# Kernel tuning notes

Hardware: AMD Instinct MI355X
Metric: run time of the kernel (lower is better)

Reference implementation:

```python
import jax, jax.numpy as jnp
import numpy as np
import math

EMBED_DIM = 64

def setup_inputs() -> dict:
    key = jax.random.key(0)
    ks = jax.random.split(key, 9)
    B, S, H, E = 2, 2048, 8, EMBED_DIM
    f16 = jnp.float16
    inp = {
        'query': jax.random.normal(ks[0], (B, S, H, E), dtype=f16),
        'key':   jax.random.normal(ks[1], (B, S, H, E), dtype=f16),
        'value': jax.random.normal(ks[2], (B, S, H, E), dtype=f16),
        # Linear params (torch Linear: y = x @ W.T + b); W stored as [out,in]
        'Wq': (jax.random.normal(ks[3], (E, E), dtype=f16) / np.float16(math.sqrt(E))),
        'bq': jax.random.normal(ks[4], (E,), dtype=f16) * np.float16(0.02),
        'Wk': (jax.random.normal(ks[5], (E, E), dtype=f16) / np.float16(math.sqrt(E))),
        'bk': jax.random.normal(ks[6], (E,), dtype=f16) * np.float16(0.02),
        'Wv': (jax.random.normal(ks[7], (E, E), dtype=f16) / np.float16(math.sqrt(E))),
        'bv': jax.random.normal(ks[8], (E,), dtype=f16) * np.float16(0.02),
    }
    return inp

def reference(query, key, value, Wq, bq, Wk, bk, Wv, bv):
    # Linear projections on last dim, fused with permute(0,2,1,3): [B,S,H,E] -> [B,H,S,E]
    q = jnp.einsum('bshe,fe->bhsf', query, Wq) + bq
    k = jnp.einsum('bshe,fe->bhsf', key, Wk) + bk
    v = jnp.einsum('bshe,fe->bhsf', value, Wv) + bv
    scale = jnp.asarray(1.0 / math.sqrt(q.shape[-1]), dtype=q.dtype)
    q = q * scale
    # full attention matrix [B,H,S,S], fp16 matmul then fp32 softmax (faithful to source)
    scores = jnp.einsum('bhse,bhte->bhst', q, k).astype(jnp.float32)
    attn = jax.nn.softmax(scores, axis=-1).astype(jnp.float16)
    out = jnp.einsum('bhst,bhte->bhse', attn, v)
    return out
```

## Files before the change

kernel.cpp:

```cpp
#include <hip/hip_runtime.h>

#define S_LEN 2048
#define NH    8
#define EMB   64
#define BM    64
#define BN    64
#define NKT   (S_LEN / BN)
#define NSPLIT 3
#define PSTR  72
#define M_INIT  (-1.0e4f)
#define EXP_CLAMP (-80.0f)

typedef _Float16 half8   __attribute__((ext_vector_type(8)));
typedef _Float16 half4   __attribute__((ext_vector_type(4)));
typedef float    float4_t __attribute__((ext_vector_type(4)));
typedef float    float8_t __attribute__((ext_vector_type(8)));

__device__ inline half8 cvt8(const float* p) {
    float8_t f = *reinterpret_cast<const float8_t*>(p);
    half8 h;
    #pragma unroll
    for (int j = 0; j < 8; ++j) h[j] = (_Float16)f[j];
    return h;
}

__device__ inline void gload_lds16(const _Float16* g, _Float16* l) {
    __builtin_amdgcn_global_load_lds(
        (const __attribute__((address_space(1))) void*)g,
        (__attribute__((address_space(3))) void*)l, 16, 0, 0);
}

__global__ __launch_bounds__(256) void proj_q(
    const float* __restrict__ X, const float* __restrict__ W,
    const float* __restrict__ bias, float* __restrict__ Out)
{
    const int tid  = threadIdx.x;
    const int lane = tid & 63;
    const int wave = tid >> 6;
    const int l15  = lane & 15;
    const int quad = lane >> 4;
    const int gwave = blockIdx.x * 4 + wave;

    half8 wf[4][2];
    #pragma unroll
    for (int ft = 0; ft < 4; ++ft)
        #pragma unroll
        for (int ks = 0; ks < 2; ++ks)
            wf[ft][ks] = cvt8(W + (ft * 16 + l15) * 64 + ks * 32 + quad * 8);
    float bv[4];
    #pragma unroll
    for (int ft = 0; ft < 4; ++ft) bv[ft] = bias[ft * 16 + l15];

    #pragma unroll
    for (int rt2 = 0; rt2 < 2; ++rt2) {
        const int rt = gwave * 2 + rt2;
        const int arow = rt * 16 + l15;
        half8 xf[2];
        #pragma unroll
        for (int ks = 0; ks < 2; ++ks)
            xf[ks] = cvt8(X + (long)arow * 64 + ks * 32 + quad * 8);
        float4_t acc[4];
        #pragma unroll
        for (int ft = 0; ft < 4; ++ft) {
            acc[ft] = (float4_t){0.f, 0.f, 0.f, 0.f};
            #pragma unroll
            for (int ks = 0; ks < 2; ++ks)
                acc[ft] = __builtin_amdgcn_mfma_f32_16x16x32_f16(
                    xf[ks], wf[ft][ks], acc[ft], 0, 0, 0);
        }
        #pragma unroll
        for (int r = 0; r < 4; ++r) {
            const int row = rt * 16 + quad * 4 + r;
            const int b = row >> 14;
            const int s = (row >> 3) & 2047;
            const int h = row & 7;
            const long orow = ((long)(b * NH + h) * S_LEN + s) * EMB;
            #pragma unroll
            for (int ft = 0; ft < 4; ++ft) {
                const _Float16 v =
                    (_Float16)(acc[ft][r] + bv[ft]) * (_Float16)0.125f;
                Out[orow + ft * 16 + l15] = (float)v;
            }
        }
    }
}

__global__ __launch_bounds__(256) void proj_kv(
    const float* __restrict__ k_in, const float* __restrict__ v_in,
    const float* __restrict__ Wk, const float* __restrict__ bk,
    const float* __restrict__ Wv, const float* __restrict__ bv_,
    _Float16* __restrict__ KT8, _Float16* __restrict__ VT8)
{
    const int seg = blockIdx.x >> 8;
    const int bid = blockIdx.x & 255;
    const float* X    = seg ? v_in : k_in;
    const float* W    = seg ? Wv : Wk;
    const float* bias = seg ? bv_ : bk;

    const int tid  = threadIdx.x;
    const int lane = tid & 63;
    const int wave = tid >> 6;
    const int l15  = lane & 15;
    const int quad = lane >> 4;
    const int gwave = bid * 4 + wave;

    half8 wf[4][2];
    #pragma unroll
    for (int ft = 0; ft < 4; ++ft)
        #pragma unroll
        for (int ks = 0; ks < 2; ++ks)
            wf[ft][ks] = cvt8(W + (ft * 16 + l15) * 64 + ks * 32 + quad * 8);
    float bv[4];
    #pragma unroll
    for (int ft = 0; ft < 4; ++ft) bv[ft] = bias[ft * 16 + l15];

    #pragma unroll
    for (int rt2 = 0; rt2 < 2; ++rt2) {
        const int rt = gwave * 2 + rt2;
        const int arow = rt * 16 + l15;
        half8 xf[2];
        #pragma unroll
        for (int ks = 0; ks < 2; ++ks)
            xf[ks] = cvt8(X + (long)arow * 64 + ks * 32 + quad * 8);
        float4_t acc[4];
        #pragma unroll
        for (int ft = 0; ft < 4; ++ft) {
            acc[ft] = (float4_t){0.f, 0.f, 0.f, 0.f};
            #pragma unroll
            for (int ks = 0; ks < 2; ++ks)
                acc[ft] = __builtin_amdgcn_mfma_f32_16x16x32_f16(
                    xf[ks], wf[ft][ks], acc[ft], 0, 0, 0);
        }
        #pragma unroll
        for (int r = 0; r < 4; ++r) {
            const int row = rt * 16 + quad * 4 + r;
            const int b = row >> 14;
            const int s = (row >> 3) & 2047;
            const int h = row & 7;
            const int bh = b * NH + h;
            #pragma unroll
            for (int ft = 0; ft < 4; ++ft) {
                const _Float16 v = (_Float16)(acc[ft][r] + bv[ft]);
                const int f = ft * 16 + l15;
                if (seg == 0)
                    KT8[(((long)bh * 8 + (f >> 3)) * S_LEN + s) * 8 + (f & 7)] = v;
                else
                    VT8[(((long)bh * 256 + (s >> 3)) * 64 + f) * 8 + (s & 7)] = v;
            }
        }
    }
}

__global__ __launch_bounds__(256, 6) void attn_part(
    const _Float16* __restrict__ KT, const _Float16* __restrict__ VT,
    const float* __restrict__ Qbuf,
    _Float16* __restrict__ p0, _Float16* __restrict__ p1,
    _Float16* __restrict__ p2, float* __restrict__ stats)
{
    __shared__ __align__(16) _Float16 Kb[8 * 64 * 8];
    __shared__ __align__(16) _Float16 Vb[8 * 64 * 8];
    __shared__ __align__(16) _Float16 Pl[4][16 * PSTR];

    const int tid  = threadIdx.x;
    const int lane = tid & 63;
    const int wave = tid >> 6;
    const int l15  = lane & 15;
    const int quad = lane >> 4;
    const int bx   = blockIdx.x;
    const int bh   = bx / (32 * NSPLIT);
    const int rem  = bx % (32 * NSPLIT);
    const int qt   = rem / NSPLIT;
    const int sp   = rem % NSPLIT;
    const long base = (long)bh * S_LEN * EMB;
    const int qrow0 = qt * BM + wave * 16;

    const _Float16* kg = KT + (long)bh * 8 * S_LEN * 8;

    half8 qf[2];
    #pragma unroll
    for (int ks = 0; ks < 2; ++ks)
        qf[ks] = cvt8(Qbuf + base + (long)(qrow0 + l15) * EMB + ks * 32 + quad * 8);

    float4_t o[4];
    #pragma unroll
    for (int et = 0; et < 4; ++et) o[et] = (float4_t){0.f, 0.f, 0.f, 0.f};
    float m_run = M_INIT, l_run = 0.f;

    const int kb = (sp * NKT) / NSPLIT, ke = ((sp + 1) * NKT) / NSPLIT;
    for (int kt = kb; kt < ke; ++kt) {
        if (kt > kb) __syncthreads();
        const int t0 = kt * BN;
        #pragma unroll
        for (int rr = 0; rr < 2; ++rr) {
            const int u = rr * 256 + tid;
            const int ec = u >> 6, tl = u & 63;
            gload_lds16(kg + ((long)ec * S_LEN + t0 + tl) * 8, Kb + u * 8);
        }
        const _Float16* vg = VT + ((long)bh * 256 + (t0 >> 3)) * 512;
        #pragma unroll
        for (int rr = 0; rr < 2; ++rr) {
            const int u = rr * 256 + tid;
            gload_lds16(vg + u * 8, Vb + u * 8);
        }
        __syncthreads();

        float4_t sacc[4];
        #pragma unroll
        for (int nt = 0; nt < 4; ++nt) sacc[nt] = (float4_t){0.f, 0.f, 0.f, 0.f};
        #pragma unroll
        for (int nt = 0; nt < 4; ++nt)
            #pragma unroll
            for (int ks = 0; ks < 2; ++ks) {
                half8 kf = *reinterpret_cast<const half8*>(
                    Kb + (ks * 4 + quad) * 512 + (nt * 16 + l15) * 8);
                sacc[nt] = __builtin_amdgcn_mfma_f32_16x16x32_f16(
                    kf, qf[ks], sacc[nt], 0, 0, 0);
            }

        float mx = sacc[0][0];
        #pragma unroll
        for (int nt = 0; nt < 4; ++nt)
            #pragma unroll
            for (int r = 0; r < 4; ++r) mx = fmaxf(mx, sacc[nt][r]);
        mx = fmaxf(mx, __shfl_xor(mx, 16));
        mx = fmaxf(mx, __shfl_xor(mx, 32));

        const float mn = fmaxf(m_run, mx);
        const float alpha = __expf(fmaxf(m_run - mn, EXP_CLAMP));
        m_run = mn;

        _Float16* Pw = Pl[wave];
        float rsum = 0.f;
        #pragma unroll
        for (int nt = 0; nt < 4; ++nt) {
            half4 ph;
            #pragma unroll
            for (int r = 0; r < 4; ++r) {
                const float p = __expf(sacc[nt][r] - m_run);
                rsum += p;
                ph[r] = (_Float16)p;
            }
            *reinterpret_cast<half4*>(&Pw[l15 * PSTR + nt * 16 + quad * 4]) = ph;
        }
        rsum += __shfl_xor(rsum, 16);
        rsum += __shfl_xor(rsum, 32);
        l_run = l_run * alpha + rsum;

        #pragma unroll
        for (int r = 0; r < 4; ++r) {
            const float ar = __shfl(alpha, quad * 4 + r);
            #pragma unroll
            for (int et = 0; et < 4; ++et) o[et][r] *= ar;
        }

        #pragma unroll
        for (int ts = 0; ts < 2; ++ts) {
            half8 pf = *reinterpret_cast<const half8*>(
                &Pw[l15 * PSTR + ts * 32 + quad * 8]);
            #pragma unroll
            for (int et = 0; et < 4; ++et) {
                half8 vf = *reinterpret_cast<const half8*>(
                    Vb + (ts * 4 + quad) * 512 + (et * 16 + l15) * 8);
                o[et] = __builtin_amdgcn_mfma_f32_16x16x32_f16(pf, vf, o[et], 0, 0, 0);
            }
        }
    }

    _Float16* pp = (sp == 0) ? p0 : (sp == 1) ? p1 : p2;
    #pragma unroll
    for (int r = 0; r < 4; ++r) {
        const float lr = __shfl(l_run, quad * 4 + r);
        const float inv = 1.f / lr;
        const int row = qrow0 + quad * 4 + r;
        const int R = bh * S_LEN + row;
        #pragma unroll
        for (int et = 0; et < 4; ++et)
            pp[(long)R * EMB + et * 16 + l15] = (_Float16)(o[et][r] * inv);
    }
    if (lane < 16) {
        const int R = bh * S_LEN + qrow0 + lane;
        stats[sp * 32768 + R] = m_run;
        stats[(NSPLIT + sp) * 32768 + R] = l_run;
    }
}

__global__ __launch_bounds__(256) void attn_combine(
    const _Float16* __restrict__ p0, const _Float16* __restrict__ p1,
    const _Float16* __restrict__ p2, const float* __restrict__ stats,
    float* __restrict__ out)
{
    const int gid = blockIdx.x * 256 + threadIdx.x;
    const int R  = gid >> 2;
    const int c0 = (gid & 3) * 16;
    const float m0 = stats[R], m1 = stats[32768 + R], m2 = stats[2 * 32768 + R];
    const float l0 = stats[3 * 32768 + R], l1 = stats[4 * 32768 + R],
                l2 = stats[5 * 32768 + R];
    const float M = fmaxf(fmaxf(m0, m1), m2);
    float w0 = l0 * __expf(fmaxf(m0 - M, EXP_CLAMP));
    float w1 = l1 * __expf(fmaxf(m1 - M, EXP_CLAMP));
    float w2 = l2 * __expf(fmaxf(m2 - M, EXP_CLAMP));
    const float rinv = 1.f / (w0 + w1 + w2);
    w0 *= rinv; w1 *= rinv; w2 *= rinv;
    const long i0 = (long)R * EMB + c0;
    #pragma unroll
    for (int h = 0; h < 2; ++h) {
        half8 a = *reinterpret_cast<const half8*>(p0 + i0 + h * 8);
        half8 b = *reinterpret_cast<const half8*>(p1 + i0 + h * 8);
        half8 c = *reinterpret_cast<const half8*>(p2 + i0 + h * 8);
        #pragma unroll
        for (int j = 0; j < 8; ++j)
            out[i0 + h * 8 + j] = (float)(_Float16)(
                w0 * (float)a[j] + w1 * (float)b[j] + w2 * (float)c[j]);
    }
}

extern "C" void kernel_launch(void* const* d_in, const int* in_sizes, int n_in,
                              void* d_out, int out_size, void* d_ws, size_t ws_size,
                              hipStream_t stream) {
    const float* q_in = (const float*)d_in[0];
    const float* k_in = (const float*)d_in[1];
    const float* v_in = (const float*)d_in[2];
    const float* Wq   = (const float*)d_in[3];
    const float* bq   = (const float*)d_in[4];
    const float* Wk   = (const float*)d_in[5];
    const float* bk   = (const float*)d_in[6];
    const float* Wv   = (const float*)d_in[7];
    const float* bv   = (const float*)d_in[8];
    float* out = (float*)d_out;

    _Float16* KT8   = (_Float16*)d_in[0];
    _Float16* VT8   = (_Float16*)((char*)d_in[0] + (4u << 20));
    _Float16* part0 = (_Float16*)d_in[2];
    _Float16* part1 = part0 + (long)2 * 1024 * 1024;
    _Float16* part2 = (_Float16*)d_in[1];
    float*    stats = (float*)((char*)d_in[1] + (4u << 20));

    proj_q<<<256, 256, 0, stream>>>(q_in, Wq, bq, out);
    proj_kv<<<512, 256, 0, stream>>>(k_in, v_in, Wk, bk, Wv, bv, KT8, VT8);
    attn_part<<<16 * 32 * NSPLIT, 256, 0, stream>>>(KT8, VT8, out,
                                                    part0, part1, part2, stats);
    attn_combine<<<512, 256, 0, stream>>>(part0, part1, part2, stats, out);
}
```

Baseline: 141.0 us.

## Double-buffer K/V tiles, defer softmax rescale, compute row sums via MFMA

```diff
diff --git a/kernel.cpp b/kernel.cpp
--- a/kernel.cpp
+++ b/kernel.cpp
@@ -4,12 +4,12 @@
 #define NH    8
 #define EMB   64
 #define BM    64
-#define BN    64
+#define BN    32
 #define NKT   (S_LEN / BN)
 #define NSPLIT 3
-#define PSTR  72
 #define M_INIT  (-1.0e4f)
 #define EXP_CLAMP (-80.0f)
+#define DEFER_THR 8.0f
 
 typedef _Float16 half8   __attribute__((ext_vector_type(8)));
 typedef _Float16 half4   __attribute__((ext_vector_type(4)));
@@ -157,130 +157,157 @@
     _Float16* __restrict__ p0, _Float16* __restrict__ p1,
     _Float16* __restrict__ p2, float* __restrict__ stats)
 {
-    __shared__ __align__(16) _Float16 Kb[8 * 64 * 8];
-    __shared__ __align__(16) _Float16 Vb[8 * 64 * 8];
-    __shared__ __align__(16) _Float16 Pl[4][16 * PSTR];
+    __shared__ __align__(16) _Float16 Kb[2][8 * 32 * 8];
+    __shared__ __align__(16) _Float16 Vb[2][4 * 64 * 8];
+    __shared__ __align__(16) _Float16 Pl[4][16 * 32];
 
     const int tid  = threadIdx.x;
     const int lane = tid & 63;
     const int wave = tid >> 6;
     const int l15  = lane & 15;
     const int quad = lane >> 4;
-    const int bx   = blockIdx.x;
-    const int bh   = bx / (32 * NSPLIT);
-    const int rem  = bx % (32 * NSPLIT);
-    const int qt   = rem / NSPLIT;
-    const int sp   = rem % NSPLIT;
+
+    const int bx     = blockIdx.x;
+    const int xcd    = bx & 7;
+    const int j      = bx >> 3;
+    const int hh     = (j >= 96) ? 1 : 0;
+    const int within = j - hh * 96;
+    const int bh     = xcd * 2 + hh;
+    const int qt     = within / NSPLIT;
+    const int sp     = within - qt * NSPLIT;
+
     const long base = (long)bh * S_LEN * EMB;
     const int qrow0 = qt * BM + wave * 16;
-
-    const _Float16* kg = KT + (long)bh * 8 * S_LEN * 8;
+    const _Float16* kg  = KT + (long)bh * 8 * S_LEN * 8;
+    const _Float16* vgh = VT + (long)bh * 256 * 512;
+
+    const _Float16* ksrc = kg + ((long)(tid >> 5) * S_LEN + (tid & 31)) * 8;
+    const _Float16* vsrc = vgh + tid * 8;
+
+    const int kb = (sp * NKT) / NSPLIT, ke = ((sp + 1) * NKT) / NSPLIT;
+    const int ntile = ke - kb;
+
+    {
+        const int t0 = kb * BN;
+        gload_lds16(ksrc + (long)t0 * 8,  &Kb[0][tid * 8]);
+        gload_lds16(vsrc + (long)t0 * 64, &Vb[0][tid * 8]);
+    }
 
     half8 qf[2];
     #pragma unroll
     for (int ks = 0; ks < 2; ++ks)
         qf[ks] = cvt8(Qbuf + base + (long)(qrow0 + l15) * EMB + ks * 32 + quad * 8);
 
+    half8 vones;
+    #pragma unroll
+    for (int jj = 0; jj < 8; ++jj) vones[jj] = (_Float16)1.0f;
+
     float4_t o[4];
     #pragma unroll
     for (int et = 0; et < 4; ++et) o[et] = (float4_t){0.f, 0.f, 0.f, 0.f};
-    float m_run = M_INIT, l_run = 0.f;
-
-    const int kb = (sp * NKT) / NSPLIT, ke = ((sp + 1) * NKT) / NSPLIT;
-    for (int kt = kb; kt < ke; ++kt) {
-        if (kt > kb) __syncthreads();
-        const int t0 = kt * BN;
-        #pragma unroll
-        for (int rr = 0; rr < 2; ++rr) {
-            const int u = rr * 256 + tid;
-            const int ec = u >> 6, tl = u & 63;
-            gload_lds16(kg + ((long)ec * S_LEN + t0 + tl) * 8, Kb + u * 8);
-        }
-        const _Float16* vg = VT + ((long)bh * 256 + (t0 >> 3)) * 512;
-        #pragma unroll
-        for (int rr = 0; rr < 2; ++rr) {
-            const int u = rr * 256 + tid;
-            gload_lds16(vg + u * 8, Vb + u * 8);
-        }
-        __syncthreads();
-
-        float4_t sacc[4];
-        #pragma unroll
-        for (int nt = 0; nt < 4; ++nt) sacc[nt] = (float4_t){0.f, 0.f, 0.f, 0.f};
-        #pragma unroll
-        for (int nt = 0; nt < 4; ++nt)
+    float4_t lacc = (float4_t){0.f, 0.f, 0.f, 0.f};
+    float m_run = M_INIT;
+
+    const int pswz = (l15 & 3) << 3;
+    _Float16* Pw = Pl[wave];
+
+    __syncthreads();
+
+    for (int it = 0; it < ntile; ++it) {
+        const int cur = it & 1;
+        const bool more = (it + 1 < ntile);
+
+        if (more) {
+            const int t0 = (kb + it + 1) * BN;
+            gload_lds16(ksrc + (long)t0 * 8,  &Kb[cur ^ 1][tid * 8]);
+            gload_lds16(vsrc + (long)t0 * 64, &Vb[cur ^ 1][tid * 8]);
+        }
+
+        const _Float16* Kc = Kb[cur];
+        const _Float16* Vc = Vb[cur];
+
+        float4_t sacc[2];
+        sacc[0] = (float4_t){0.f, 0.f, 0.f, 0.f};
+        sacc[1] = (float4_t){0.f, 0.f, 0.f, 0.f};
+        __builtin_amdgcn_s_setprio(1);
+        #pragma unroll
+        for (int nt = 0; nt < 2; ++nt)
             #pragma unroll
             for (int ks = 0; ks < 2; ++ks) {
                 half8 kf = *reinterpret_cast<const half8*>(
-                    Kb + (ks * 4 + quad) * 512 + (nt * 16 + l15) * 8);
+                    Kc + (ks * 4 + quad) * 256 + (nt * 16 + l15) * 8);
                 sacc[nt] = __builtin_amdgcn_mfma_f32_16x16x32_f16(
                     kf, qf[ks], sacc[nt], 0, 0, 0);
             }
-
-        float mx = sacc[0][0];
-        #pragma unroll
-        for (int nt = 0; nt < 4; ++nt)
-            #pragma unroll
-            for (int r = 0; r < 4; ++r) mx = fmaxf(mx, sacc[nt][r]);
-        mx = fmaxf(mx, __shfl_xor(mx, 16));
-        mx = fmaxf(mx, __shfl_xor(mx, 32));
-
-        const float mn = fmaxf(m_run, mx);
-        const float alpha = __expf(fmaxf(m_run - mn, EXP_CLAMP));
-        m_run = mn;
-
-        _Float16* Pw = Pl[wave];
-        float rsum = 0.f;
-        #pragma unroll
-        for (int nt = 0; nt < 4; ++nt) {
+        __builtin_amdgcn_s_setprio(0);
+
+        float mx = fmaxf(fmaxf(sacc[0][0], sacc[0][1]), sacc[0][2]);
+        mx = fmaxf(fmaxf(mx, sacc[0][3]), sacc[1][0]);
+        mx = fmaxf(fmaxf(mx, sacc[1][1]), sacc[1][2]);
+        mx = fmaxf(mx, sacc[1][3]);
+
+        if (!__all(mx - m_run <= DEFER_THR)) {
+            float mr = fmaxf(mx, __shfl_xor(mx, 16));
+            mr = fmaxf(mr, __shfl_xor(mr, 32));
+            const float mn = fmaxf(m_run, mr);
+            const float alpha = __expf(fmaxf(m_run - mn, EXP_CLAMP));
+            m_run = mn;
+            #pragma unroll
+            for (int r = 0; r < 4; ++r) {
+                const float ar = __shfl(alpha, quad * 4 + r);
+                lacc[r] *= ar;
+                #pragma unroll
+                for (int et = 0; et < 4; ++et) o[et][r] *= ar;
+            }
+        }
+
+        #pragma unroll
+        for (int nt = 0; nt < 2; ++nt) {
             half4 ph;
             #pragma unroll
-            for (int r = 0; r < 4; ++r) {
-                const float p = __expf(sacc[nt][r] - m_run);
-                rsum += p;
-                ph[r] = (_Float16)p;
-            }
-            *reinterpret_cast<half4*>(&Pw[l15 * PSTR + nt * 16 + quad * 4]) = ph;
-        }
-        rsum += __shfl_xor(rsum, 16);
-        rsum += __shfl_xor(rsum, 32);
-        l_run = l_run * alpha + rsum;
-
-        #pragma unroll
-        for (int r = 0; r < 4; ++r) {
-            const float ar = __shfl(alpha, quad * 4 + r);
-            #pragma unroll
-            for (int et = 0; et < 4; ++et) o[et][r] *= ar;
-        }
-
-        #pragma unroll
-        for (int ts = 0; ts < 2; ++ts) {
-            half8 pf = *reinterpret_cast<const half8*>(
-                &Pw[l15 * PSTR + ts * 32 + quad * 8]);
-            #pragma unroll
-            for (int et = 0; et < 4; ++et) {
-                half8 vf = *reinterpret_cast<const half8*>(
-                    Vb + (ts * 4 + quad) * 512 + (et * 16 + l15) * 8);
-                o[et] = __builtin_amdgcn_mfma_f32_16x16x32_f16(pf, vf, o[et], 0, 0, 0);
-            }
-        }
+            for (int r = 0; r < 4; ++r)
+                ph[r] = (_Float16)__expf(sacc[nt][r] - m_run);
+            *reinterpret_cast<half4*>(
+                &Pw[l15 * 32 + ((nt * 16 + quad * 4) ^ pswz)]) = ph;
+        }
+        half8 pf = *reinterpret_cast<const half8*>(
+            &Pw[l15 * 32 + ((quad * 8) ^ pswz)]);
+        __builtin_amdgcn_s_setprio(1);
+        #pragma unroll
+        for (int et = 0; et < 4; ++et) {
+            half8 vf = *reinterpret_cast<const half8*>(
+                Vc + quad * 512 + (et * 16 + l15) * 8);
+            o[et] = __builtin_amdgcn_mfma_f32_16x16x32_f16(pf, vf, o[et], 0, 0, 0);
+        }
+        lacc = __builtin_amdgcn_mfma_f32_16x16x32_f16(pf, vones, lacc, 0, 0, 0);
+        __builtin_amdgcn_s_setprio(0);
+
+        if (more) __syncthreads();
     }
 
     _Float16* pp = (sp == 0) ? p0 : (sp == 1) ? p1 : p2;
     #pragma unroll
     for (int r = 0; r < 4; ++r) {
-        const float lr = __shfl(l_run, quad * 4 + r);
-        const float inv = 1.f / lr;
+        const float inv = 1.f / lacc[r];
         const int row = qrow0 + quad * 4 + r;
         const int R = bh * S_LEN + row;
         #pragma unroll
         for (int et = 0; et < 4; ++et)
             pp[(long)R * EMB + et * 16 + l15] = (_Float16)(o[et][r] * inv);
     }
-    if (lane < 16) {
-        const int R = bh * S_LEN + qrow0 + lane;
-        stats[sp * 32768 + R] = m_run;
-        stats[(NSPLIT + sp) * 32768 + R] = l_run;
+    {
+        const int srcl = (lane >> 2) * 16;
+        const float s0 = __shfl(lacc[0], srcl);
+        const float s1 = __shfl(lacc[1], srcl);
+        const float s2 = __shfl(lacc[2], srcl);
+        const float s3 = __shfl(lacc[3], srcl);
+        const int rr = lane & 3;
+        const float lsel = (rr == 0) ? s0 : (rr == 1) ? s1 : (rr == 2) ? s2 : s3;
+        if (lane < 16) {
+            const int R = bh * S_LEN + qrow0 + lane;
+            stats[sp * 32768 + R] = m_run;
+            stats[(NSPLIT + sp) * 32768 + R] = lsel;
+        }
     }
 }
 
```

Result: no change. 143.5 us (+1.8%).
